# Kernel optimization log

Hardware: AMD Instinct MI355X
Metric: run time of the kernel (lower is better)

The kernel has to match this reference:

```python
import jax, jax.numpy as jnp
import numpy as np

NUM_HEADS = 16
ROPE_BASE = 10000.0


def _rope_cos_sin(seq_len, head_dim, dtype):
    inv_freq = 1.0 / (ROPE_BASE ** (jnp.arange(0, head_dim, 2, dtype=jnp.float32) / head_dim))
    t = jnp.arange(seq_len, dtype=jnp.float32)
    freqs = jnp.einsum('i,j->ij', t, inv_freq)            # [S, hd/2]
    emb = jnp.concatenate((freqs, freqs), axis=-1)         # [S, hd]
    return emb.astype(dtype).cos if False else (jnp.cos(emb).astype(dtype), jnp.sin(emb).astype(dtype))


def _rotate_half(x):
    x1, x2 = jnp.split(x, 2, axis=-1)
    return jnp.concatenate((-x2, x1), axis=-1)


def setup_inputs() -> dict:
    key = jax.random.key(0)
    ks = jax.random.split(key, 5)
    B, S, D = 2, 2048, 2048
    x = jax.random.normal(ks[0], (B, S, D), dtype=jnp.float32)
    sc = 1.0 / np.sqrt(D)
    Wq = jax.random.normal(ks[1], (D, D), dtype=jnp.float32) * sc
    Wk = jax.random.normal(ks[2], (D, D), dtype=jnp.float32) * sc
    Wv = jax.random.normal(ks[3], (D, D), dtype=jnp.float32) * sc
    Wo = jax.random.normal(ks[4], (D, D), dtype=jnp.float32) * sc
    mask = jnp.tril(jnp.ones((S, S), dtype=bool))[None, None]  # causal [1,1,S,S]
    return {"x": x, "Wq": Wq, "Wk": Wk, "Wv": Wv, "Wo": Wo, "mask": mask}


def reference(x, Wq, Wk, Wv, Wo, mask):
    B, S, D = x.shape
    H = NUM_HEADS
    hd = D // H
    scale = hd ** -0.5

    def split_heads(t):
        return t.reshape(B, S, H, hd).transpose(0, 2, 1, 3)  # [B,H,S,hd]

    q = split_heads(x @ Wq.T)
    k = split_heads(x @ Wk.T)
    v = split_heads(x @ Wv.T)

    cos, sin = _rope_cos_sin(S, hd, x.dtype)                 # [S,hd]
    cos = cos[None, None]
    sin = sin[None, None]
    q = q * cos + _rotate_half(q) * sin
    k = k * cos + _rotate_half(k) * sin

    scores = jnp.einsum('bhqd,bhkd->bhqk', q, k) * scale
    scores = jnp.where(mask, scores, jnp.finfo(scores.dtype).min)
    attn = jax.nn.softmax(scores, axis=-1)                    # dropout p applied in eval mode -> identity
    out = jnp.einsum('bhqk,bhkd->bhqd', attn, v)
    out = out.transpose(0, 2, 1, 3).reshape(B, S, D)
    return out @ Wo.T
```

## Files before the change

### kernel.cpp

```cpp
#include <hip/hip_runtime.h>
#include <math.h>

#define S_LEN 2048
#define D_MODEL 2048
#define NHEADS 16
#define HDIM 128
#define BATCH 2
#define MTOT (BATCH * S_LEN)

typedef unsigned short u16;
typedef __attribute__((ext_vector_type(8))) short short8;
typedef __attribute__((ext_vector_type(4))) float floatx4;
typedef __attribute__((ext_vector_type(4))) float float4v;

__device__ __forceinline__ u16 f2bf(float f) {
    union { float f; unsigned u; } v; v.f = f;
    unsigned r = v.u + 0x7fff + ((v.u >> 16) & 1);
    return (u16)(r >> 16);
}
__device__ __forceinline__ float bf2f(u16 b) {
    union { unsigned u; float f; } v; v.u = ((unsigned)b) << 16;
    return v.f;
}

__device__ __forceinline__ void gl_lds16(const void* g, void* l) {
    __builtin_amdgcn_global_load_lds(
        (const __attribute__((address_space(1))) unsigned int*)g,
        (__attribute__((address_space(3))) unsigned int*)l, 16, 0, 0);
}

__global__ void convert_in(const float* __restrict__ src, u16* __restrict__ dst) {
    int t = blockIdx.x * blockDim.x + threadIdx.x;
    float4v a = ((const float4v*)src)[t * 2];
    float4v b = ((const float4v*)src)[t * 2 + 1];
    union { short8 v; u16 e[8]; } o;
    o.e[0] = f2bf(a[0]); o.e[1] = f2bf(a[1]); o.e[2] = f2bf(a[2]); o.e[3] = f2bf(a[3]);
    o.e[4] = f2bf(b[0]); o.e[5] = f2bf(b[1]); o.e[6] = f2bf(b[2]); o.e[7] = f2bf(b[3]);
    *(short8*)(dst + (size_t)t * 8) = o.v;
}

__global__ __launch_bounds__(256, 2) void gemm_nt(const u16* __restrict__ A,
                                                  const u16* __restrict__ W,
                                                  u16* __restrict__ Cb,
                                                  float* __restrict__ Cf,
                                                  int K) {
    __shared__ __align__(16) u16 lA[128 * 64];
    __shared__ __align__(16) u16 lB[128 * 64];
    const int tid = threadIdx.x;
    const int wave = tid >> 6, lane = tid & 63;
    const int l15 = lane & 15, quad = lane >> 4;
    const int mtile = blockIdx.y * 128;
    const int ntile = blockIdx.x * 128;
    const int wm = (wave >> 1) * 64, wn = (wave & 1) * 64;

    floatx4 acc[4][4] = {};

    for (int k0 = 0; k0 < K; k0 += 64) {
        __syncthreads();
#pragma unroll
        for (int i = 0; i < 4; ++i) {
            int slot = i * 256 + tid;
            int row = slot >> 3, kc = slot & 7;
            gl_lds16(A + (size_t)(mtile + row) * K + k0 + kc * 8,
                     &lA[(size_t)(i * 256 + wave * 64) * 8]);
            gl_lds16(W + (size_t)(ntile + row) * K + k0 + kc * 8,
                     &lB[(size_t)(i * 256 + wave * 64) * 8]);
        }
        __syncthreads();
#pragma unroll
        for (int ks = 0; ks < 2; ++ks) {
            short8 af[4], bf[4];
#pragma unroll
            for (int rf = 0; rf < 4; ++rf)
                af[rf] = *(const short8*)&lA[(wm + rf * 16 + l15) * 64 + ks * 32 + quad * 8];
#pragma unroll
            for (int cf = 0; cf < 4; ++cf)
                bf[cf] = *(const short8*)&lB[(wn + cf * 16 + l15) * 64 + ks * 32 + quad * 8];
#pragma unroll
            for (int rf = 0; rf < 4; ++rf)
#pragma unroll
                for (int cf = 0; cf < 4; ++cf)
                    acc[rf][cf] = __builtin_amdgcn_mfma_f32_16x16x32_bf16(
                        af[rf], bf[cf], acc[rf][cf], 0, 0, 0);
        }
    }
#pragma unroll
    for (int rf = 0; rf < 4; ++rf)
#pragma unroll
        for (int cf = 0; cf < 4; ++cf)
#pragma unroll
            for (int r = 0; r < 4; ++r) {
                size_t row = mtile + wm + rf * 16 + quad * 4 + r;
                size_t col = ntile + wn + cf * 16 + l15;
                if (Cb) Cb[row * D_MODEL + col] = f2bf(acc[rf][cf][r]);
                else    Cf[row * D_MODEL + col] = acc[rf][cf][r];
            }
}

__global__ void rope_kernel(u16* __restrict__ Q, u16* __restrict__ Kb) {
    int idx = blockIdx.x * blockDim.x + threadIdx.x;
    int jg = idx & 7;
    int h = (idx >> 3) & 15;
    int token = idx >> 7;
    int s = token & (S_LEN - 1);
    size_t base = (size_t)token * D_MODEL + h * HDIM + jg * 8;
    union { short8 v; u16 e[8]; } q1, q2, k1, k2, oq1, oq2, ok1, ok2;
    q1.v = *(const short8*)(Q + base);  q2.v = *(const short8*)(Q + base + 64);
    k1.v = *(const short8*)(Kb + base); k2.v = *(const short8*)(Kb + base + 64);
#pragma unroll
    for (int e = 0; e < 8; ++e) {
        int j = jg * 8 + e;
        float invf = exp2f(-(float)j * 0.20762050593046995f);
        float ang = (float)s * invf;
        float c = cosf(ang), sn = sinf(ang);
        float a = bf2f(q1.e[e]), b = bf2f(q2.e[e]);
        oq1.e[e] = f2bf(a * c - b * sn);
        oq2.e[e] = f2bf(b * c + a * sn);
        float ka = bf2f(k1.e[e]), kb2 = bf2f(k2.e[e]);
        ok1.e[e] = f2bf(ka * c - kb2 * sn);
        ok2.e[e] = f2bf(kb2 * c + ka * sn);
    }
    *(short8*)(Q + base) = oq1.v;  *(short8*)(Q + base + 64) = oq2.v;
    *(short8*)(Kb + base) = ok1.v; *(short8*)(Kb + base + 64) = ok2.v;
}

__global__ void transpose_v(const u16* __restrict__ V, u16* __restrict__ Vt) {
    __shared__ u16 t[64][66];
    int b = blockIdx.z;
    int s0 = blockIdx.x * 64;
    int c0 = blockIdx.y * 64;
    int tid = threadIdx.x;
#pragma unroll
    for (int i = 0; i < 2; ++i) {
        int slot = i * 256 + tid;
        int r = slot >> 3, cc = slot & 7;
        union { short8 v; u16 a[8]; } u;
        u.v = *(const short8*)(V + (size_t)(b * S_LEN + s0 + r) * D_MODEL + c0 + cc * 8);
#pragma unroll
        for (int e = 0; e < 8; ++e) t[r][cc * 8 + e] = u.a[e];
    }
    __syncthreads();
#pragma unroll
    for (int i = 0; i < 2; ++i) {
        int slot = i * 256 + tid;
        int d = slot >> 3, sc = slot & 7;
        union { short8 v; u16 a[8]; } o;
#pragma unroll
        for (int e = 0; e < 8; ++e) o.a[e] = t[sc * 8 + e][d];
        int col = c0 + d;
        int h = col >> 7, dd = col & 127;
        u16* dst = Vt + ((size_t)((b * NHEADS + h) * HDIM + dd)) * S_LEN + s0 + sc * 8;
        *(short8*)dst = o.v;
    }
}

__global__ __launch_bounds__(256, 2) void flash_attn(const u16* __restrict__ Q,
                                                     const u16* __restrict__ Kb,
                                                     const u16* __restrict__ Vt,
                                                     u16* __restrict__ O) {
    __shared__ __align__(16) u16 lK[128 * 128];
    __shared__ __align__(16) u16 lV[128 * 128];
    const int bid = blockIdx.x;
    const int qt = bid & 15;
    const int bh = bid >> 4;
    const int h = bh & 15;
    const int b = bh >> 4;
    const int tid = threadIdx.x;
    const int wave = tid >> 6, lane = tid & 63;
    const int l15 = lane & 15, quad = lane >> 4;
    const int qbase = qt * 128;
    const int wrow = wave * 32;

    short8 qf[2][4];
#pragma unroll
    for (int rf = 0; rf < 2; ++rf)
#pragma unroll
        for (int ks = 0; ks < 4; ++ks)
            qf[rf][ks] = *(const short8*)(Q +
                (size_t)(b * S_LEN + qbase + wrow + rf * 16 + l15) * D_MODEL +
                h * HDIM + ks * 32 + quad * 8);

    floatx4 oacc[2][8] = {};
    float mrow[2][4], lrow[2][4];
#pragma unroll
    for (int rf = 0; rf < 2; ++rf)
#pragma unroll
        for (int r = 0; r < 4; ++r) { mrow[rf][r] = -1e30f; lrow[rf][r] = 0.f; }

    const float scale = 0.08838834764831845f;

    for (int kt = 0; kt <= qt; ++kt) {
        const int kbase = kt * 128;
        __syncthreads();
#pragma unroll
        for (int i = 0; i < 8; ++i) {
            int slot = i * 256 + tid;
            int row = slot >> 4, sc = slot & 15;
            gl_lds16(Kb + (size_t)(b * S_LEN + kbase + row) * D_MODEL + h * HDIM + sc * 8,
                     &lK[(size_t)(i * 256 + wave * 64) * 8]);
            gl_lds16(Vt + ((size_t)(bh * HDIM + row)) * S_LEN + kbase + sc * 8,
                     &lV[(size_t)(i * 256 + wave * 64) * 8]);
        }
        __syncthreads();

        floatx4 sacc[2][8] = {};
#pragma unroll
        for (int ks = 0; ks < 4; ++ks) {
            short8 kf[8];
#pragma unroll
            for (int cf = 0; cf < 8; ++cf)
                kf[cf] = *(const short8*)&lK[(cf * 16 + l15) * 128 + ks * 32 + quad * 8];
#pragma unroll
            for (int rf = 0; rf < 2; ++rf)
#pragma unroll
                for (int cf = 0; cf < 8; ++cf)
                    sacc[rf][cf] = __builtin_amdgcn_mfma_f32_16x16x32_bf16(
                        qf[rf][ks], kf[cf], sacc[rf][cf], 0, 0, 0);
        }

        const bool diag = (kt == qt);
#pragma unroll
        for (int rf = 0; rf < 2; ++rf) {
#pragma unroll
            for (int r = 0; r < 4; ++r) {
                const int qrow = wrow + rf * 16 + quad * 4 + r;
                float vmax = -1e30f;
#pragma unroll
                for (int cf = 0; cf < 8; ++cf) {
                    float sv = sacc[rf][cf][r] * scale;
                    if (diag && (cf * 16 + l15) > qrow) sv = -1e30f;
                    sacc[rf][cf][r] = sv;
                    vmax = fmaxf(vmax, sv);
                }
#pragma unroll
                for (int m = 8; m >= 1; m >>= 1)
                    vmax = fmaxf(vmax, __shfl_xor(vmax, m, 16));
                float mnew = fmaxf(mrow[rf][r], vmax);
                float alpha = __expf(mrow[rf][r] - mnew);
                mrow[rf][r] = mnew;
                float rsum = 0.f;
#pragma unroll
                for (int cf = 0; cf < 8; ++cf) {
                    float p = __expf(sacc[rf][cf][r] - mnew);
                    sacc[rf][cf][r] = p;
                    rsum += p;
                }
#pragma unroll
                for (int m = 8; m >= 1; m >>= 1) rsum += __shfl_xor(rsum, m, 16);
                lrow[rf][r] = lrow[rf][r] * alpha + rsum;
#pragma unroll
                for (int cf = 0; cf < 8; ++cf) oacc[rf][cf][r] *= alpha;
            }
        }

        __syncthreads();
        u16* pbuf = &lK[(size_t)wave * 32 * 128];
#pragma unroll
        for (int rf = 0; rf < 2; ++rf)
#pragma unroll
            for (int cf = 0; cf < 8; ++cf)
#pragma unroll
                for (int r = 0; r < 4; ++r)
                    pbuf[(rf * 16 + quad * 4 + r) * 128 + cf * 16 + l15] =
                        f2bf(sacc[rf][cf][r]);
        __syncthreads();
#pragma unroll
        for (int ks = 0; ks < 4; ++ks) {
            short8 pf[2], vf[8];
#pragma unroll
            for (int rf = 0; rf < 2; ++rf)
                pf[rf] = *(const short8*)&pbuf[(rf * 16 + l15) * 128 + ks * 32 + quad * 8];
#pragma unroll
            for (int cf = 0; cf < 8; ++cf)
                vf[cf] = *(const short8*)&lV[(cf * 16 + l15) * 128 + ks * 32 + quad * 8];
#pragma unroll
            for (int rf = 0; rf < 2; ++rf)
#pragma unroll
                for (int cf = 0; cf < 8; ++cf)
                    oacc[rf][cf] = __builtin_amdgcn_mfma_f32_16x16x32_bf16(
                        pf[rf], vf[cf], oacc[rf][cf], 0, 0, 0);
        }
    }

#pragma unroll
    for (int rf = 0; rf < 2; ++rf)
#pragma unroll
        for (int r = 0; r < 4; ++r) {
            float inv = 1.0f / lrow[rf][r];
            int row = qbase + wrow + rf * 16 + quad * 4 + r;
#pragma unroll
            for (int cf = 0; cf < 8; ++cf) {
                int col = h * HDIM + cf * 16 + l15;
                O[(size_t)(b * S_LEN + row) * D_MODEL + col] = f2bf(oacc[rf][cf][r] * inv);
            }
        }
}

extern "C" void kernel_launch(void* const* d_in, const int* in_sizes, int n_in,
                              void* d_out, int out_size, void* d_ws, size_t ws_size,
                              hipStream_t stream) {
    const float* x  = (const float*)d_in[0];
    const float* Wq = (const float*)d_in[1];
    const float* Wk = (const float*)d_in[2];
    const float* Wv = (const float*)d_in[3];
    const float* Wo = (const float*)d_in[4];
    float* out = (float*)d_out;

    const size_t NX = (size_t)MTOT * D_MODEL;
    const size_t NW = (size_t)D_MODEL * D_MODEL;
    u16* base = (u16*)d_ws;
    u16* Qb  = base;
    u16* Kb  = base + NX;
    u16* Vb  = base + 2 * NX;
    u16* xb  = base + 3 * NX;
    u16* Vt  = xb;
    u16* Hb  = base + 4 * NX;
    u16* wqb = Kb;
    u16* wkb = Vb;
    u16* Ob  = Qb;

    dim3 blk(256);
    hipLaunchKernelGGL(convert_in, dim3(NX / 2048), blk, 0, stream, x,  xb);
    hipLaunchKernelGGL(convert_in, dim3(NW / 2048), blk, 0, stream, Wq, wqb);
    hipLaunchKernelGGL(convert_in, dim3(NW / 2048), blk, 0, stream, Wk, wkb);
    hipLaunchKernelGGL(convert_in, dim3(NW / 2048), blk, 0, stream, Wv, Hb);

    dim3 gg(D_MODEL / 128, MTOT / 128);
    hipLaunchKernelGGL(gemm_nt, gg, blk, 0, stream, xb, wqb, Qb, (float*)nullptr, D_MODEL);
    hipLaunchKernelGGL(gemm_nt, gg, blk, 0, stream, xb, wkb, Kb, (float*)nullptr, D_MODEL);
    hipLaunchKernelGGL(gemm_nt, gg, blk, 0, stream, xb, Hb,  Vb, (float*)nullptr, D_MODEL);
    hipLaunchKernelGGL(convert_in, dim3(NW / 2048), blk, 0, stream, Wo, Hb);
    hipLaunchKernelGGL(rope_kernel, dim3((MTOT * NHEADS * 8) / 256), blk, 0, stream, Qb, Kb);
    hipLaunchKernelGGL(transpose_v, dim3(S_LEN / 64, D_MODEL / 64, BATCH), blk, 0, stream, Vb, Vt);
    hipLaunchKernelGGL(flash_attn, dim3(BATCH * NHEADS * (S_LEN / 128)), blk, 0, stream,
                       Qb, Kb, Vt, Ob);
    hipLaunchKernelGGL(gemm_nt, gg, blk, 0, stream, Ob, Hb, (u16*)nullptr, out, D_MODEL);
}
```

Baseline: 590.3 us.

## Double-buffer K/V tiles with XOR-swizzled LDS in flash attention

Splits each 128-key tile into two 64-key sub-tiles held in ping-pong LDS buffers, so loading the next K/V tile through global_load_lds overlaps with compute on the current one. Explicit vmcnt waits and raw s_barrier calls replace __syncthreads. K, V and P are stored with an XOR swizzle on 16-byte chunks to cut LDS bank conflicts. The cost is more loop iterations, each with a smaller MFMA workload, and more delicate hand-written synchronization.

```diff
diff --git a/kernel.cpp b/kernel.cpp
--- a/kernel.cpp
+++ b/kernel.cpp
@@ -27,6 +27,13 @@
     __builtin_amdgcn_global_load_lds(
         (const __attribute__((address_space(1))) unsigned int*)g,
         (__attribute__((address_space(3))) unsigned int*)l, 16, 0, 0);
+}
+
+__device__ __forceinline__ int swzA(int row, int col) {
+    return row * 128 + (((col >> 3) ^ (row & 7)) << 3) + (col & 7);
+}
+__device__ __forceinline__ int swzB(int row, int col) {
+    return row * 64 + (((col >> 3) ^ (row & 7)) << 3) + (col & 7);
 }
 
 __global__ void convert_in(const float* __restrict__ src, u16* __restrict__ dst) {
@@ -158,8 +165,10 @@
                                                      const u16* __restrict__ Kb,
                                                      const u16* __restrict__ Vt,
                                                      u16* __restrict__ O) {
-    __shared__ __align__(16) u16 lK[128 * 128];
-    __shared__ __align__(16) u16 lV[128 * 128];
+    __shared__ __align__(16) u16 lK0[64 * 128];
+    __shared__ __align__(16) u16 lK1[64 * 128];
+    __shared__ __align__(16) u16 lV0[128 * 64];
+    __shared__ __align__(16) u16 lV1[128 * 64];
     const int bid = blockIdx.x;
     const int qt = bid & 15;
     const int bh = bid >> 4;
@@ -188,37 +197,62 @@
         for (int r = 0; r < 4; ++r) { mrow[rf][r] = -1e30f; lrow[rf][r] = 0.f; }
 
     const float scale = 0.08838834764831845f;
-
-    for (int kt = 0; kt <= qt; ++kt) {
-        const int kbase = kt * 128;
-        __syncthreads();
-#pragma unroll
-        for (int i = 0; i < 8; ++i) {
-            int slot = i * 256 + tid;
-            int row = slot >> 4, sc = slot & 15;
-            gl_lds16(Kb + (size_t)(b * S_LEN + kbase + row) * D_MODEL + h * HDIM + sc * 8,
-                     &lK[(size_t)(i * 256 + wave * 64) * 8]);
-            gl_lds16(Vt + ((size_t)(bh * HDIM + row)) * S_LEN + kbase + sc * 8,
-                     &lV[(size_t)(i * 256 + wave * 64) * 8]);
-        }
-        __syncthreads();
-
-        floatx4 sacc[2][8] = {};
+    const int NT = 2 * (qt + 1);
+
+#define STAGE_KV(dK, dV, kb_)                                                   \
+    {                                                                           \
+        _Pragma("unroll")                                                       \
+        for (int i = 0; i < 4; ++i) {                                           \
+            int slot = i * 256 + tid;                                           \
+            int krow = slot >> 4, ksc = slot & 15;                              \
+            int kssc = ksc ^ (krow & 7);                                        \
+            gl_lds16(Kb + (size_t)(b * S_LEN + (kb_) + krow) * D_MODEL +        \
+                         h * HDIM + kssc * 8,                                   \
+                     (dK) + (size_t)(i * 256 + wave * 64) * 8);                 \
+            int vrow = slot >> 3, vsc = slot & 7;                               \
+            int vssc = vsc ^ (vrow & 7);                                        \
+            gl_lds16(Vt + ((size_t)(bh * HDIM + vrow)) * S_LEN + (kb_) +        \
+                         vssc * 8,                                              \
+                     (dV) + (size_t)(i * 256 + wave * 64) * 8);                 \
+        }                                                                       \
+    }
+
+    STAGE_KV(lK0, lV0, 0);
+
+    for (int kt2 = 0; kt2 < NT; ++kt2) {
+        u16* cK = (kt2 & 1) ? lK1 : lK0;
+        u16* cV = (kt2 & 1) ? lV1 : lV0;
+        u16* nK = (kt2 & 1) ? lK0 : lK1;
+        u16* nV = (kt2 & 1) ? lV0 : lV1;
+        const int kbase = kt2 * 64;
+
+        if (kt2 + 1 < NT) {
+            STAGE_KV(nK, nV, kbase + 64);
+            asm volatile("s_waitcnt vmcnt(8)" ::: "memory");
+        } else {
+            asm volatile("s_waitcnt vmcnt(0)" ::: "memory");
+        }
+        __builtin_amdgcn_sched_barrier(0);
+        __builtin_amdgcn_s_barrier();
+        __builtin_amdgcn_sched_barrier(0);
+
+        floatx4 sacc[2][4] = {};
 #pragma unroll
         for (int ks = 0; ks < 4; ++ks) {
-            short8 kf[8];
-#pragma unroll
-            for (int cf = 0; cf < 8; ++cf)
-                kf[cf] = *(const short8*)&lK[(cf * 16 + l15) * 128 + ks * 32 + quad * 8];
+            short8 kf[4];
+#pragma unroll
+            for (int cf = 0; cf < 4; ++cf)
+                kf[cf] = *(const short8*)&cK[swzA(cf * 16 + l15, ks * 32 + quad * 8)];
 #pragma unroll
             for (int rf = 0; rf < 2; ++rf)
 #pragma unroll
-                for (int cf = 0; cf < 8; ++cf)
+                for (int cf = 0; cf < 4; ++cf)
                     sacc[rf][cf] = __builtin_amdgcn_mfma_f32_16x16x32_bf16(
                         qf[rf][ks], kf[cf], sacc[rf][cf], 0, 0, 0);
         }
 
-        const bool diag = (kt == qt);
+        const bool diag = (kt2 >= 2 * qt);
+        const int coff = kbase - qbase;
 #pragma unroll
         for (int rf = 0; rf < 2; ++rf) {
 #pragma unroll
@@ -226,9 +260,9 @@
                 const int qrow = wrow + rf * 16 + quad * 4 + r;
                 float vmax = -1e30f;
 #pragma unroll
-                for (int cf = 0; cf < 8; ++cf) {
+                for (int cf = 0; cf < 4; ++cf) {
                     float sv = sacc[rf][cf][r] * scale;
-                    if (diag && (cf * 16 + l15) > qrow) sv = -1e30f;
+                    if (diag && (coff + cf * 16 + l15) > qrow) sv = -1e30f;
                     sacc[rf][cf][r] = sv;
                     vmax = fmaxf(vmax, sv);
                 }
@@ -240,7 +274,7 @@
                 mrow[rf][r] = mnew;
                 float rsum = 0.f;
 #pragma unroll
-                for (int cf = 0; cf < 8; ++cf) {
+                for (int cf = 0; cf < 4; ++cf) {
                     float p = __expf(sacc[rf][cf][r] - mnew);
                     sacc[rf][cf][r] = p;
                     rsum += p;
@@ -253,26 +287,30 @@
             }
         }
 
-        __syncthreads();
-        u16* pbuf = &lK[(size_t)wave * 32 * 128];
+        asm volatile("s_waitcnt lgkmcnt(0)" ::: "memory");
+        __builtin_amdgcn_sched_barrier(0);
+        __builtin_amdgcn_s_barrier();
+        __builtin_amdgcn_sched_barrier(0);
+
+        u16* pbuf = cK + (size_t)wave * 32 * 64;
 #pragma unroll
         for (int rf = 0; rf < 2; ++rf)
 #pragma unroll
+            for (int cf = 0; cf < 4; ++cf)
+#pragma unroll
+                for (int r = 0; r < 4; ++r)
+                    pbuf[swzB(rf * 16 + quad * 4 + r, cf * 16 + l15)] =
+                        f2bf(sacc[rf][cf][r]);
+
+#pragma unroll
+        for (int ks2 = 0; ks2 < 2; ++ks2) {
+            short8 pf[2], vf[8];
+#pragma unroll
+            for (int rf = 0; rf < 2; ++rf)
+                pf[rf] = *(const short8*)&pbuf[swzB(rf * 16 + l15, ks2 * 32 + quad * 8)];
+#pragma unroll
             for (int cf = 0; cf < 8; ++cf)
-#pragma unroll
-                for (int r = 0; r < 4; ++r)
-                    pbuf[(rf * 16 + quad * 4 + r) * 128 + cf * 16 + l15] =
-                        f2bf(sacc[rf][cf][r]);
-        __syncthreads();
-#pragma unroll
-        for (int ks = 0; ks < 4; ++ks) {
-            short8 pf[2], vf[8];
-#pragma unroll
-            for (int rf = 0; rf < 2; ++rf)
-                pf[rf] = *(const short8*)&pbuf[(rf * 16 + l15) * 128 + ks * 32 + quad * 8];
-#pragma unroll
-            for (int cf = 0; cf < 8; ++cf)
-                vf[cf] = *(const short8*)&lV[(cf * 16 + l15) * 128 + ks * 32 + quad * 8];
+                vf[cf] = *(const short8*)&cV[swzB(cf * 16 + l15, ks2 * 32 + quad * 8)];
 #pragma unroll
             for (int rf = 0; rf < 2; ++rf)
 #pragma unroll
@@ -280,7 +318,13 @@
                     oacc[rf][cf] = __builtin_amdgcn_mfma_f32_16x16x32_bf16(
                         pf[rf], vf[cf], oacc[rf][cf], 0, 0, 0);
         }
-    }
+
+        asm volatile("s_waitcnt lgkmcnt(0)" ::: "memory");
+        __builtin_amdgcn_sched_barrier(0);
+        __builtin_amdgcn_s_barrier();
+        __builtin_amdgcn_sched_barrier(0);
+    }
+#undef STAGE_KV
 
 #pragma unroll
     for (int rf = 0; rf < 2; ++rf)
```

Measured after the change: 526.7 us. 10.8% less time.
